# Optimization experiments

Measured on AMD Instinct MI355X. Metric: run time of the kernel, lower is better.

## Reference

```python
import jax, jax.numpy as jnp
import numpy as np

N_ITEMS = 200000
EMB = 100
LAYERS = 3
N_EDGES = 6400000


def setup_inputs() -> dict:
    key = jax.random.key(0)
    k1, k2, k3, k4, k5 = jax.random.split(key, 5)
    embedding = jax.random.normal(k1, (N_ITEMS, EMB), dtype=jnp.float32)
    adj_vals = jax.random.uniform(k2, (N_EDGES,), dtype=jnp.float32)
    weights = jax.random.normal(k3, (LAYERS, EMB, EMB), dtype=jnp.float32) * (1.0 / np.sqrt(EMB))
    adj_rows = jax.random.randint(k4, (N_EDGES,), 0, N_ITEMS, dtype=jnp.int32)
    adj_cols = jax.random.randint(k5, (N_EDGES,), 0, N_ITEMS, dtype=jnp.int32)
    return {"embedding": embedding, "adj_vals": adj_vals, "weights": weights,
            "adj_rows": adj_rows, "adj_cols": adj_cols}


def reference(embedding, adj_vals, weights, adj_rows, adj_cols):
    # embedding: [N, d]; weights: [L, d, d] (torch Linear weight, y = x @ W.T)
    # adjacency in COO: out[r] += v * x[c]
    n = embedding.shape[0]
    eps = 1e-12  # F.normalize eps
    x = embedding
    finals = [x]  # layer-0 copy is NOT normalized (matches original)
    for i in range(weights.shape[0]):
        x = jnp.einsum('nd,ed->ne', x, weights[i])          # linear, no bias
        gathered = adj_vals[:, None] * x[adj_cols]           # [E, d]
        x = jax.ops.segment_sum(gathered, adj_rows, num_segments=n)  # SpMM
        norm = jnp.maximum(jnp.linalg.norm(x, axis=-1, keepdims=True), eps)
        finals.append(x / norm)  # appended copy normalized; carried x stays raw
    return jnp.mean(jnp.stack(finals, axis=0), axis=0)
```

## Files before the change

kernel.cpp:

```cpp
#include <hip/hip_runtime.h>

#define EMB 100
#define EMB2 50
#define XSTRIDE 52
#define Y8DW 32
#define BSHIFT 8
#define BROWS 256
#define MAXBUCK 1024
#define CHUNK 8192

typedef __attribute__((ext_vector_type(8))) short short8;
typedef __attribute__((ext_vector_type(4))) float f32x4;
typedef __attribute__((ext_vector_type(2))) float f2v;

__device__ __forceinline__ unsigned packbf(float a, float b) {
    unsigned ua = __float_as_uint(a), ub = __float_as_uint(b);
    unsigned ra = (ua + 0x7FFFu + ((ua >> 16) & 1u)) >> 16;
    unsigned rb = (ub + 0x7FFFu + ((ub >> 16) & 1u)) >> 16;
    return ra | (rb << 16);
}

__device__ __forceinline__ unsigned char f32_to_fp8(float f) {
#if __has_builtin(__builtin_amdgcn_cvt_pk_fp8_f32)
    return (unsigned char)(__builtin_amdgcn_cvt_pk_fp8_f32(f, f, 0, false) & 0xFF);
#else
    unsigned u = __float_as_uint(f);
    unsigned s = (u >> 24) & 0x80u;
    unsigned mag = u & 0x7FFFFFFFu;
    if (mag >= 0x43E00000u) return (unsigned char)(s | 0x7Eu);
    if (mag < 0x3C800000u) {
        int r = __float2int_rn(__uint_as_float(mag) * 512.f);
        return (unsigned char)(s | (unsigned)r);
    }
    unsigned r = mag + 0x7FFFFu + ((mag >> 20) & 1u);
    unsigned e = r >> 23, m = (r >> 20) & 7u;
    return (unsigned char)(s | ((e - 120u) << 3) | m);
#endif
}

__device__ __forceinline__ void fma_fp8x4(unsigned g, float v,
                                          float& a0, float& a1, float& a2, float& a3) {
#if __has_builtin(__builtin_amdgcn_cvt_pk_f32_fp8)
    f2v lo = __builtin_amdgcn_cvt_pk_f32_fp8((int)g, false);
    f2v hi = __builtin_amdgcn_cvt_pk_f32_fp8((int)g, true);
    a0 = fmaf(v, lo[0], a0); a1 = fmaf(v, lo[1], a1);
    a2 = fmaf(v, hi[0], a2); a3 = fmaf(v, hi[1], a3);
#else
    float o[4];
#pragma unroll
    for (int d = 0; d < 4; ++d) {
        unsigned b = (g >> (8 * d)) & 0xFFu;
        unsigned e = (b >> 3) & 15u, m = b & 7u;
        float val = e ? __uint_as_float(((e + 120u) << 23) | (m << 20))
                      : (float)m * (1.f / 512.f);
        o[d] = (b & 0x80u) ? -val : val;
    }
    a0 = fmaf(v, o[0], a0); a1 = fmaf(v, o[1], a1);
    a2 = fmaf(v, o[2], a2); a3 = fmaf(v, o[3], a3);
#endif
}

__global__ __launch_bounds__(256) void k_bucket_count(const int* __restrict__ rows,
                                                      int* __restrict__ gcnt,
                                                      int E, int nbuck) {
    __shared__ int hist[MAXBUCK];
    int tid = threadIdx.x;
    int base = blockIdx.x * CHUNK;
    for (int s = tid; s < nbuck; s += 256) hist[s] = 0;
    __syncthreads();
#pragma unroll
    for (int k = 0; k < CHUNK / 256; ++k) {
        int i = base + tid + k * 256;
        if (i < E) atomicAdd(&hist[rows[i] >> BSHIFT], 1);
    }
    __syncthreads();
    for (int s = tid; s < nbuck; s += 256)
        if (hist[s]) atomicAdd(&gcnt[s], hist[s]);
}

__global__ __launch_bounds__(1024) void k_scan2(int* __restrict__ bsum, int nb) {
    __shared__ int tmp[1024];
    int v = (threadIdx.x < nb) ? bsum[threadIdx.x] : 0;
    tmp[threadIdx.x] = v;
    __syncthreads();
    for (int off = 1; off < 1024; off <<= 1) {
        int t = (threadIdx.x >= off) ? tmp[threadIdx.x - off] : 0;
        __syncthreads();
        tmp[threadIdx.x] += t;
        __syncthreads();
    }
    if (threadIdx.x < nb) bsum[threadIdx.x] = tmp[threadIdx.x] - v;
}

__global__ __launch_bounds__(256) void k_partition(const int* __restrict__ rows,
                                                   const int* __restrict__ cols,
                                                   const float* __restrict__ vals,
                                                   int* __restrict__ bucket_next,
                                                   int2* __restrict__ part,
                                                   int E, int nbuck) {
    __shared__ int hist[MAXBUCK];
    __shared__ int base_s[MAXBUCK];
    __shared__ int cnt2[MAXBUCK];
    int tid = threadIdx.x;
    int base = blockIdx.x * CHUNK;
    for (int s = tid; s < nbuck; s += 256) hist[s] = 0;
    __syncthreads();
#pragma unroll
    for (int k = 0; k < CHUNK / 256; ++k) {
        int i = base + tid + k * 256;
        if (i < E) atomicAdd(&hist[rows[i] >> BSHIFT], 1);
    }
    __syncthreads();
    for (int s = tid; s < nbuck; s += 256) {
        if (hist[s]) base_s[s] = atomicAdd(&bucket_next[s], hist[s]);
        cnt2[s] = 0;
    }
    __syncthreads();
#pragma unroll
    for (int k = 0; k < CHUNK / 256; ++k) {
        int i = base + tid + k * 256;
        if (i < E) {
            int r = rows[i];
            int b = r >> BSHIFT;
            unsigned q = (unsigned)__float2int_rn(vals[i] * 16383.f);
            unsigned cv = (unsigned)cols[i] | (q << 18);
            int rank = atomicAdd(&cnt2[b], 1);
            part[base_s[b] + rank] = make_int2(r, (int)cv);
        }
    }
}

__global__ __launch_bounds__(256) void k_build_csr(const int2* __restrict__ part,
                                                   const int* __restrict__ bucket_end,
                                                   int* __restrict__ row_ptr,
                                                   unsigned* __restrict__ csr,
                                                   int N, int E) {
    __shared__ int cnt[BROWS];
    __shared__ int scn[BROWS];
    __shared__ int cur[BROWS];
    int b = blockIdx.x;
    int tid = threadIdx.x;
    int seg_beg = (b == 0) ? 0 : bucket_end[b - 1];
    int seg_end = bucket_end[b];
    int rowbase = b << BSHIFT;

    cnt[tid] = 0;
    __syncthreads();
    for (int i = seg_beg + tid; i < seg_end; i += 256)
        atomicAdd(&cnt[part[i].x - rowbase], 1);
    __syncthreads();
    int v = cnt[tid];
    scn[tid] = v;
    __syncthreads();
    for (int off = 1; off < 256; off <<= 1) {
        int t = (tid >= off) ? scn[tid - off] : 0;
        __syncthreads();
        scn[tid] += t;
        __syncthreads();
    }
    int rp = seg_beg + scn[tid] - v;
    if (rowbase + tid < N) row_ptr[rowbase + tid] = rp;
    cur[tid] = rp;
    if (b == 0 && tid == 0) row_ptr[N] = E;
    __syncthreads();
    for (int i = seg_beg + tid; i < seg_end; i += 256) {
        int2 e = part[i];
        int pos = atomicAdd(&cur[e.x - rowbase], 1);
        csr[pos] = (unsigned)e.y;
    }
}

template <bool F32SRC>
__global__ __launch_bounds__(256) void k_gemm_mfma(const void* __restrict__ Xv,
                                                   const float* __restrict__ W,
                                                   unsigned char* __restrict__ Y8,
                                                   int nTiles, int N) {
    __shared__ uint4 Bf[28][64];
    int tid = threadIdx.x;
#pragma unroll
    for (int it = 0; it < 7; ++it) {
        int id = it * 256 + tid;
        int fs = id >> 6, lane = id & 63;
        int nt = fs >> 2, ks = fs & 3;
        int e = nt * 16 + (lane & 15);
        int dbase = ks * 32 + (lane >> 4) * 8;
        float w[8];
#pragma unroll
        for (int j = 0; j < 8; ++j) {
            int d = dbase + j;
            w[j] = (e < EMB && d < EMB) ? W[e * EMB + d] : 0.f;
        }
        uint4 u;
        u.x = packbf(w[0], w[1]); u.y = packbf(w[2], w[3]);
        u.z = packbf(w[4], w[5]); u.w = packbf(w[6], w[7]);
        Bf[fs][lane] = u;
    }
    __syncthreads();

    int wid = (blockIdx.x * 256 + tid) >> 6;
    int nWaves = gridDim.x * 4;
    int lane = tid & 63;
    int m = lane & 15, kg = lane >> 4;

    for (int tile = wid; tile < nTiles; tile += nWaves) {
        int rowbase = tile * 16;
        int arow = rowbase + m; if (arow >= N) arow = N - 1;
        uint4 a[4];
        if (F32SRC) {
            const float* xr = (const float*)Xv + (size_t)arow * EMB;
#pragma unroll
            for (int ks = 0; ks < 3; ++ks) {
                float4 v0 = *(const float4*)(xr + ks * 32 + kg * 8);
                float4 v1 = *(const float4*)(xr + ks * 32 + kg * 8 + 4);
                a[ks] = make_uint4(packbf(v0.x, v0.y), packbf(v0.z, v0.w),
                                   packbf(v1.x, v1.y), packbf(v1.z, v1.w));
            }
            uint4 t = make_uint4(0, 0, 0, 0);
            if (kg == 0) { float4 v = *(const float4*)(xr + 96);
                           t.x = packbf(v.x, v.y); t.y = packbf(v.z, v.w); }
            a[3] = t;
        } else {
            const unsigned* xr = (const unsigned*)Xv + (size_t)arow * XSTRIDE;
#pragma unroll
            for (int ks = 0; ks < 3; ++ks)
                a[ks] = *(const uint4*)(xr + ks * 16 + kg * 4);
            uint4 t = make_uint4(0, 0, 0, 0);
            if (kg == 0) { uint2 v = *(const uint2*)(xr + 48); t.x = v.x; t.y = v.y; }
            a[3] = t;
        }

        f32x4 acc[7];
#pragma unroll
        for (int nt = 0; nt < 7; ++nt) acc[nt] = (f32x4){0.f, 0.f, 0.f, 0.f};
#pragma unroll
        for (int ks = 0; ks < 4; ++ks) {
            short8 av = __builtin_bit_cast(short8, a[ks]);
#pragma unroll
            for (int nt = 0; nt < 7; ++nt) {
                short8 bv = __builtin_bit_cast(short8, Bf[nt * 4 + ks][lane]);
                acc[nt] = __builtin_amdgcn_mfma_f32_16x16x32_bf16(av, bv, acc[nt], 0, 0, 0);
            }
        }
#pragma unroll
        for (int nt = 0; nt < 7; ++nt) {
            int e = nt * 16 + m;
            if (e < EMB) {
#pragma unroll
                for (int r = 0; r < 4; ++r) {
                    int rr = rowbase + kg * 4 + r;
                    if (rr < N)
                        Y8[((size_t)rr << 7) + e] = f32_to_fp8(acc[nt][r]);
                }
            }
        }
    }
}

__global__ __launch_bounds__(256) void k_spmm_norm(const int* __restrict__ row_ptr,
                                                   const unsigned* __restrict__ csr,
                                                   const unsigned* __restrict__ Y8,
                                                   unsigned* __restrict__ Xout,
                                                   float* __restrict__ Out,
                                                   const float* __restrict__ prev,
                                                   float pscale, float scale,
                                                   int writeX, int N) {
    int wave = (blockIdx.x * 256 + threadIdx.x) >> 6;
    int lane = threadIdx.x & 63;
    if (wave >= N) return;
    int half = lane >> 5, sub = lane & 31;
    int beg = row_ptr[wave], end = row_ptr[wave + 1];
    const float dq = 1.0f / 16383.f;
    float a0 = 0.f, a1 = 0.f, a2 = 0.f, a3 = 0.f;
    if (sub < 25) {
        const unsigned* yb = Y8 + sub;
        int j = beg + half;
        for (; j + 6 < end; j += 8) {
            unsigned u0 = __builtin_nontemporal_load(&csr[j + 0]);
            unsigned u1 = __builtin_nontemporal_load(&csr[j + 2]);
            unsigned u2 = __builtin_nontemporal_load(&csr[j + 4]);
            unsigned u3 = __builtin_nontemporal_load(&csr[j + 6]);
            unsigned g0 = yb[(u0 & 0x3FFFFu) << 5];
            unsigned g1 = yb[(u1 & 0x3FFFFu) << 5];
            unsigned g2 = yb[(u2 & 0x3FFFFu) << 5];
            unsigned g3 = yb[(u3 & 0x3FFFFu) << 5];
            float v0 = (float)(u0 >> 18) * dq;
            float v1 = (float)(u1 >> 18) * dq;
            float v2 = (float)(u2 >> 18) * dq;
            float v3 = (float)(u3 >> 18) * dq;
            fma_fp8x4(g0, v0, a0, a1, a2, a3);
            fma_fp8x4(g1, v1, a0, a1, a2, a3);
            fma_fp8x4(g2, v2, a0, a1, a2, a3);
            fma_fp8x4(g3, v3, a0, a1, a2, a3);
        }
        for (; j < end; j += 2) {
            unsigned u = csr[j];
            unsigned g = yb[(u & 0x3FFFFu) << 5];
            float v = (float)(u >> 18) * dq;
            fma_fp8x4(g, v, a0, a1, a2, a3);
        }
    }
    a0 += __shfl_xor(a0, 32, 64);
    a1 += __shfl_xor(a1, 32, 64);
    a2 += __shfl_xor(a2, 32, 64);
    a3 += __shfl_xor(a3, 32, 64);
    float ss = fmaf(a0, a0, fmaf(a1, a1, fmaf(a2, a2, a3 * a3)));
#pragma unroll
    for (int off = 16; off; off >>= 1) ss += __shfl_xor(ss, off, 64);
    float sc = scale / fmaxf(sqrtf(ss), 1e-12f);
    if (half == 0 && sub < 25) {
        if (writeX) {
            uint2 xw;
            xw.x = packbf(a0, a1); xw.y = packbf(a2, a3);
            *(uint2*)(Xout + (size_t)wave * XSTRIDE + sub * 2) = xw;
        }
        const float4* pp = (const float4*)(prev + (size_t)wave * EMB) + sub;
        float4 p = *pp;
        float4 o;
        o.x = fmaf(a0, sc, p.x * pscale);
        o.y = fmaf(a1, sc, p.y * pscale);
        o.z = fmaf(a2, sc, p.z * pscale);
        o.w = fmaf(a3, sc, p.w * pscale);
        *((float4*)(Out + (size_t)wave * EMB) + sub) = o;
    }
}

extern "C" void kernel_launch(void* const* d_in, const int* in_sizes, int n_in,
                              void* d_out, int out_size, void* d_ws, size_t ws_size,
                              hipStream_t stream) {
    const float* emb   = (const float*)d_in[0];
    const float* avals = (const float*)d_in[1];
    const float* wts   = (const float*)d_in[2];
    const int*   arows = (const int*)d_in[3];
    const int*   acols = (const int*)d_in[4];

    const int N = in_sizes[0] / EMB;
    const int E = in_sizes[1];
    const int L = in_sizes[2] / (EMB * EMB);
    const float scale = 1.0f / (float)(L + 1);
    const int nbuck = (N + BROWS - 1) >> BSHIFT;

    unsigned* Y8     = (unsigned*)d_ws;
    unsigned* bufX   = Y8 + (size_t)N * Y8DW;
    int* row_ptr     = (int*)(bufX + (size_t)N * XSTRIDE);
    int* bucket_next = row_ptr + (N + 2);
    unsigned* csr    = (unsigned*)(bucket_next + MAXBUCK);
    int2* part       = (int2*)d_ws;
    float* out = (float*)d_out;

    const int nchunk = (E + CHUNK - 1) / CHUNK;

    hipMemsetAsync(bucket_next, 0, MAXBUCK * sizeof(int), stream);
    k_bucket_count<<<nchunk, 256, 0, stream>>>(arows, bucket_next, E, nbuck);
    k_scan2<<<1, 1024, 0, stream>>>(bucket_next, nbuck);
    k_partition<<<nchunk, 256, 0, stream>>>(arows, acols, avals, bucket_next,
                                            part, E, nbuck);
    k_build_csr<<<nbuck, 256, 0, stream>>>(part, bucket_next, row_ptr, csr, N, E);

    const int nTiles = (N + 15) / 16;
    const int gemm_blocks = 782;
    const int spmm_blocks = (N + 3) / 4;

    k_gemm_mfma<true><<<gemm_blocks, 256, 0, stream>>>(emb, wts,
                                                       (unsigned char*)Y8, nTiles, N);
    k_spmm_norm<<<spmm_blocks, 256, 0, stream>>>(row_ptr, csr, Y8, bufX,
                                                 out, emb, scale, scale, 1, N);
    for (int l = 1; l < L; ++l) {
        k_gemm_mfma<false><<<gemm_blocks, 256, 0, stream>>>(
            bufX, wts + (size_t)l * EMB * EMB, (unsigned char*)Y8, nTiles, N);
        k_spmm_norm<<<spmm_blocks, 256, 0, stream>>>(row_ptr, csr, Y8, bufX,
                                                     out, out, 1.0f, scale,
                                                     (l < L - 1) ? 1 : 0, N);
    }
}
```

Before: 977.4 us.

## Pack GEMM fp8 stores into dwords, deepen SpMM gather unroll, enlarge partition chunks

The GEMM swaps the MFMA operand order so each lane holds four consecutive output columns of one row. It then packs them into a single 32-bit fp8 word with the paired convert builtin, replacing scattered byte stores. The SpMM inner loop now issues 8 independent gathers per iteration instead of 4, for more memory-level parallelism. The partition kernels use 4x larger chunks with partial unrolling, giving fewer blocks and fewer global atomics. The cost is higher register pressure and less parallelism in the preprocessing kernels.

```diff
diff --git a/kernel.cpp b/kernel.cpp
--- a/kernel.cpp
+++ b/kernel.cpp
@@ -7,7 +7,7 @@
 #define BSHIFT 8
 #define BROWS 256
 #define MAXBUCK 1024
-#define CHUNK 8192
+#define CHUNK 32768
 
 typedef __attribute__((ext_vector_type(8))) short short8;
 typedef __attribute__((ext_vector_type(4))) float f32x4;
@@ -21,9 +21,6 @@
 }
 
 __device__ __forceinline__ unsigned char f32_to_fp8(float f) {
-#if __has_builtin(__builtin_amdgcn_cvt_pk_fp8_f32)
-    return (unsigned char)(__builtin_amdgcn_cvt_pk_fp8_f32(f, f, 0, false) & 0xFF);
-#else
     unsigned u = __float_as_uint(f);
     unsigned s = (u >> 24) & 0x80u;
     unsigned mag = u & 0x7FFFFFFFu;
@@ -35,6 +32,15 @@
     unsigned r = mag + 0x7FFFFu + ((mag >> 20) & 1u);
     unsigned e = r >> 23, m = (r >> 20) & 7u;
     return (unsigned char)(s | ((e - 120u) << 3) | m);
+}
+
+__device__ __forceinline__ unsigned pack4_fp8(float a0, float a1, float a2, float a3) {
+#if __has_builtin(__builtin_amdgcn_cvt_pk_fp8_f32)
+    int lo = __builtin_amdgcn_cvt_pk_fp8_f32(a0, a1, 0, false);
+    return (unsigned)__builtin_amdgcn_cvt_pk_fp8_f32(a2, a3, lo, true);
+#else
+    return (unsigned)f32_to_fp8(a0) | ((unsigned)f32_to_fp8(a1) << 8) |
+           ((unsigned)f32_to_fp8(a2) << 16) | ((unsigned)f32_to_fp8(a3) << 24);
 #endif
 }
 
@@ -68,7 +74,7 @@
     int base = blockIdx.x * CHUNK;
     for (int s = tid; s < nbuck; s += 256) hist[s] = 0;
     __syncthreads();
-#pragma unroll
+#pragma unroll 4
     for (int k = 0; k < CHUNK / 256; ++k) {
         int i = base + tid + k * 256;
         if (i < E) atomicAdd(&hist[rows[i] >> BSHIFT], 1);
@@ -105,7 +111,7 @@
     int base = blockIdx.x * CHUNK;
     for (int s = tid; s < nbuck; s += 256) hist[s] = 0;
     __syncthreads();
-#pragma unroll
+#pragma unroll 4
     for (int k = 0; k < CHUNK / 256; ++k) {
         int i = base + tid + k * 256;
         if (i < E) atomicAdd(&hist[rows[i] >> BSHIFT], 1);
@@ -116,7 +122,7 @@
         cnt2[s] = 0;
     }
     __syncthreads();
-#pragma unroll
+#pragma unroll 4
     for (int k = 0; k < CHUNK / 256; ++k) {
         int i = base + tid + k * 256;
         if (i < E) {
@@ -173,7 +179,7 @@
 template <bool F32SRC>
 __global__ __launch_bounds__(256) void k_gemm_mfma(const void* __restrict__ Xv,
                                                    const float* __restrict__ W,
-                                                   unsigned char* __restrict__ Y8,
+                                                   unsigned* __restrict__ Y8,
                                                    int nTiles, int N) {
     __shared__ uint4 Bf[28][64];
     int tid = threadIdx.x;
@@ -238,20 +244,17 @@
 #pragma unroll
             for (int nt = 0; nt < 7; ++nt) {
                 short8 bv = __builtin_bit_cast(short8, Bf[nt * 4 + ks][lane]);
-                acc[nt] = __builtin_amdgcn_mfma_f32_16x16x32_bf16(av, bv, acc[nt], 0, 0, 0);
+                acc[nt] = __builtin_amdgcn_mfma_f32_16x16x32_bf16(bv, av, acc[nt], 0, 0, 0);
             }
         }
-#pragma unroll
-        for (int nt = 0; nt < 7; ++nt) {
-            int e = nt * 16 + m;
-            if (e < EMB) {
-#pragma unroll
-                for (int r = 0; r < 4; ++r) {
-                    int rr = rowbase + kg * 4 + r;
-                    if (rr < N)
-                        Y8[((size_t)rr << 7) + e] = f32_to_fp8(acc[nt][r]);
-                }
-            }
+        int rr = rowbase + m;
+        if (rr < N) {
+            unsigned* yrow = Y8 + ((size_t)rr << 5) + kg;
+#pragma unroll
+            for (int nt = 0; nt < 6; ++nt)
+                yrow[nt * 4] = pack4_fp8(acc[nt][0], acc[nt][1], acc[nt][2], acc[nt][3]);
+            if (kg == 0)
+                yrow[24] = pack4_fp8(acc[6][0], acc[6][1], acc[6][2], acc[6][3]);
         }
     }
 }
@@ -274,29 +277,34 @@
     if (sub < 25) {
         const unsigned* yb = Y8 + sub;
         int j = beg + half;
+        for (; j + 14 < end; j += 16) {
+            unsigned u[8], g[8];
+#pragma unroll
+            for (int t = 0; t < 8; ++t)
+                u[t] = __builtin_nontemporal_load(&csr[j + 2 * t]);
+#pragma unroll
+            for (int t = 0; t < 8; ++t)
+                g[t] = yb[(u[t] & 0x3FFFFu) << 5];
+#pragma unroll
+            for (int t = 0; t < 8; ++t)
+                fma_fp8x4(g[t], (float)(u[t] >> 18) * dq, a0, a1, a2, a3);
+        }
         for (; j + 6 < end; j += 8) {
-            unsigned u0 = __builtin_nontemporal_load(&csr[j + 0]);
-            unsigned u1 = __builtin_nontemporal_load(&csr[j + 2]);
-            unsigned u2 = __builtin_nontemporal_load(&csr[j + 4]);
-            unsigned u3 = __builtin_nontemporal_load(&csr[j + 6]);
-            unsigned g0 = yb[(u0 & 0x3FFFFu) << 5];
-            unsigned g1 = yb[(u1 & 0x3FFFFu) << 5];
-            unsigned g2 = yb[(u2 & 0x3FFFFu) << 5];
-            unsigned g3 = yb[(u3 & 0x3FFFFu) << 5];
-            float v0 = (float)(u0 >> 18) * dq;
-            float v1 = (float)(u1 >> 18) * dq;
-            float v2 = (float)(u2 >> 18) * dq;
-            float v3 = (float)(u3 >> 18) * dq;
-            fma_fp8x4(g0, v0, a0, a1, a2, a3);
-            fma_fp8x4(g1, v1, a0, a1, a2, a3);
-            fma_fp8x4(g2, v2, a0, a1, a2, a3);
-            fma_fp8x4(g3, v3, a0, a1, a2, a3);
+            unsigned u[4], g[4];
+#pragma unroll
+            for (int t = 0; t < 4; ++t)
+                u[t] = __builtin_nontemporal_load(&csr[j + 2 * t]);
+#pragma unroll
+            for (int t = 0; t < 4; ++t)
+                g[t] = yb[(u[t] & 0x3FFFFu) << 5];
+#pragma unroll
+            for (int t = 0; t < 4; ++t)
+                fma_fp8x4(g[t], (float)(u[t] >> 18) * dq, a0, a1, a2, a3);
         }
         for (; j < end; j += 2) {
             unsigned u = csr[j];
             unsigned g = yb[(u & 0x3FFFFu) << 5];
-            float v = (float)(u >> 18) * dq;
-            fma_fp8x4(g, v, a0, a1, a2, a3);
+            fma_fp8x4(g, (float)(u >> 18) * dq, a0, a1, a2, a3);
         }
     }
     a0 += __shfl_xor(a0, 32, 64);
@@ -360,13 +368,12 @@
     const int gemm_blocks = 782;
     const int spmm_blocks = (N + 3) / 4;
 
-    k_gemm_mfma<true><<<gemm_blocks, 256, 0, stream>>>(emb, wts,
-                                                       (unsigned char*)Y8, nTiles, N);
+    k_gemm_mfma<true><<<gemm_blocks, 256, 0, stream>>>(emb, wts, Y8, nTiles, N);
     k_spmm_norm<<<spmm_blocks, 256, 0, stream>>>(row_ptr, csr, Y8, bufX,
                                                  out, emb, scale, scale, 1, N);
     for (int l = 1; l < L; ++l) {
         k_gemm_mfma<false><<<gemm_blocks, 256, 0, stream>>>(
-            bufX, wts + (size_t)l * EMB * EMB, (unsigned char*)Y8, nTiles, N);
+            bufX, wts + (size_t)l * EMB * EMB, Y8, nTiles, N);
         k_spmm_norm<<<spmm_blocks, 256, 0, stream>>>(row_ptr, csr, Y8, bufX,
                                                      out, out, 1.0f, scale,
                                                      (l < L - 1) ? 1 : 0, N);
```

New measurement: 904.0 us. 7.5% less time.
